# Performance work log

Hardware: AMD Instinct MI355X
Metric: run time of the kernel (lower is better)

The kernel has to match this reference:

```python
import jax, jax.numpy as jnp
import numpy as np

SR = 16000
FRAME_LENGTH = 2048
HOP = 512
WIN_LENGTH = 30
FREQ_LOW = 85
FREQ_HIGH = 3400
EPS = 1e-9


def setup_inputs() -> dict:
    key = jax.random.key(0)
    waveform = jax.random.normal(key, (8, 960000), dtype=jnp.float32)
    return {"waveform": waveform}


def _detect_pitch(w):
    # w: [B, T] padded waveform. Mirrors torchaudio.functional.detect_pitch_frequency.
    B, T = w.shape
    frame_size = int(np.ceil(SR * (HOP / SR)))          # = HOP = 512
    lags = int(np.ceil(SR / FREQ_LOW))                  # 189
    num_frames = int(np.ceil(T / frame_size))
    p = lags + num_frames * frame_size - T
    wp = jnp.pad(w, ((0, 0), (0, p)))                   # [B, lags + F*fs]
    frames = wp[:, : num_frames * frame_size].reshape(B, num_frames, frame_size)
    s1n = (EPS + jnp.linalg.norm(frames, axis=-1)) ** 2  # [B, F], lag-independent

    def body(carry, lag):
        seg = jax.lax.dynamic_slice_in_dim(wp, lag, num_frames * frame_size, axis=1)
        seg = seg.reshape(B, num_frames, frame_size)
        num = jnp.sum(frames * seg, axis=-1)
        s2n = (EPS + jnp.linalg.norm(seg, axis=-1)) ** 2
        return carry, num / s1n / s2n

    _, nccf = jax.lax.scan(body, None, jnp.arange(1, lags + 1))  # [lags, B, F]
    nccf = jnp.moveaxis(nccf, 0, -1)                             # [B, F, lags]

    # _find_max_per_frame
    lag_min = int(np.ceil(SR / FREQ_HIGH))  # 5
    half_size = lags // 2                   # 94
    best_v = jnp.max(nccf[..., lag_min:], axis=-1)
    best_i = jnp.argmax(nccf[..., lag_min:], axis=-1)
    half_v = jnp.max(nccf[..., lag_min:half_size], axis=-1)
    half_i = jnp.argmax(nccf[..., lag_min:half_size], axis=-1)
    mask = half_v > 0.99 * best_v           # prefer near-max with smallest lag
    idx = jnp.where(mask, half_i, best_i) + lag_min + 1  # +1 calibration offset

    # lower median (sorted index (n-1)//2). Output length = F - (WIN_LENGTH-1-pad_len).
    pad_len = (WIN_LENGTH - 1) // 2         # 14
    padded = jnp.concatenate([jnp.tile(idx[:, :1], (1, pad_len)), idx], axis=-1)
    out_len = padded.shape[-1] - WIN_LENGTH + 1
    win_idx = jnp.arange(out_len)[:, None] + jnp.arange(WIN_LENGTH)[None, :]
    wins = padded[:, win_idx]               # [B, out_len, WIN_LENGTH]
    med = jnp.sort(wins, axis=-1)[..., (WIN_LENGTH - 1) // 2]

    return SR / (EPS + med.astype(jnp.float32))


def reference(waveform):
    pad = FRAME_LENGTH // 2
    wpad = jnp.pad(waveform, ((0, 0), (pad, pad)), mode="reflect")
    pitch = _detect_pitch(wpad)
    desired = waveform.shape[-1] // HOP + 1
    if pitch.shape[-1] > desired:
        pitch = pitch[..., :desired]
    else:
        pitch = jnp.pad(pitch, ((0, 0), (0, desired - pitch.shape[-1])))
    return pitch
```

## Files before the change

kernel.cpp:

```cpp
#include <hip/hip_runtime.h>

#define T_WPAD  962048
#define T_RAW   960000
#define NFRM    1879
#define OUTW    1876
#define MEDLEN  1864
#define WINL    30
#define PADL    14
#define FPB     8
#define NBX     235
#define XLEN    4296

__global__ __launch_bounds__(256) void nccf_kernel(const float* __restrict__ wav,
                                                   int* __restrict__ idxArr) {
    const int bx   = blockIdx.x;
    const int b    = blockIdx.y;
    const int tid  = threadIdx.x;
    const int wave = tid >> 6;
    const int lane = tid & 63;
    const int h    = lane >> 5;
    const int s    = lane & 31;

    __shared__ __align__(16) float X[XLEN];
    __shared__ float Pw1[FPB][190];
    __shared__ float Pw2[FPB][190];

    const long a0 = (long)bx * (FPB * 512);
    const float* wrow = wav + (long)b * T_RAW;

    for (int i = tid; i < XLEN; i += 256) {
        float v = 0.0f;
        long t = a0 + i;
        if (t < T_WPAD) {
            long u = t - 1024;
            if (u < 0) u = -u;
            if (u >= T_RAW) u = 2L * (T_RAW - 1) - u;
            v = wrow[u];
        }
        X[i] = v;
    }
    __syncthreads();

    const int F = wave * 2 + h;
    const int g = bx * FPB + F;
    const bool valid = (g < NFRM);
    const float* Xf = X + F * 512;

    {
        const float* p = Xf + s * 22;
        double run = 0.0;
        #pragma unroll
        for (int m = 0; m < 22; ++m) { double x = (double)p[m]; run = fma(x, x, run); }
        double inc = run;
        #pragma unroll
        for (int off = 1; off < 32; off <<= 1) {
            double v = __shfl_up(inc, off, 32);
            if (s >= off) inc += v;
        }
        double run2 = inc - run;
        #pragma unroll
        for (int m = 0; m < 22; ++m) {
            double x = (double)p[m];
            run2 = fma(x, x, run2);
            int idx = s * 22 + m + 1;
            float val = (float)run2;
            if (idx <= 189)                     Pw1[F][idx - 1]   = val;
            else if (idx >= 512 && idx <= 701)  Pw2[F][idx - 512] = val;
        }
    }

    float acc[6] = {0.f, 0.f, 0.f, 0.f, 0.f, 0.f};
    {
        const float2* X2 = (const float2*)X;
        const int base2 = (F * 512 + 6 * s) >> 1;
        float w[12];
        #pragma unroll
        for (int d = 0; d < 6; ++d) {
            float2 t2 = X2[base2 + d];
            w[2 * d] = t2.x; w[2 * d + 1] = t2.y;
        }
        const float4* A4 = (const float4*)(X + F * 512);
        #pragma unroll 4
        for (int k = 0; k < 127; ++k) {
            float4 Av = A4[k];
            #pragma unroll
            for (int r = 0; r < 6; ++r) {
                acc[r] = fmaf(Av.x, w[1 + r], acc[r]);
                acc[r] = fmaf(Av.y, w[2 + r], acc[r]);
                acc[r] = fmaf(Av.z, w[3 + r], acc[r]);
                acc[r] = fmaf(Av.w, w[4 + r], acc[r]);
            }
            float2 n0 = X2[base2 + 2 * k + 6];
            float2 n1 = X2[base2 + 2 * k + 7];
            #pragma unroll
            for (int i = 0; i < 8; ++i) w[i] = w[i + 4];
            w[8] = n0.x; w[9] = n0.y; w[10] = n1.x; w[11] = n1.y;
        }
        {
            float4 Av = A4[127];
            #pragma unroll
            for (int r = 0; r < 6; ++r) {
                acc[r] = fmaf(Av.x, w[1 + r], acc[r]);
                acc[r] = fmaf(Av.y, w[2 + r], acc[r]);
                acc[r] = fmaf(Av.z, w[3 + r], acc[r]);
                acc[r] = fmaf(Av.w, w[4 + r], acc[r]);
            }
        }
    }

    float bestv = -1e30f, halfv = -1e30f;
    int bestk = 1 << 30, halfk = 1 << 30;
    {
        float s1 = 1e-9f + sqrtf(Pw2[F][0]);
        float s1n = s1 * s1;
        #pragma unroll
        for (int r = 0; r < 6; ++r) {
            int lag  = 6 * s + 1 + r;
            int kidx = lag - 1;
            if (kidx <= 188) {
                float q  = Pw2[F][lag] - Pw1[F][lag - 1];
                float s2 = 1e-9f + sqrtf(q);
                float v  = acc[r] / s1n / (s2 * s2);
                if (kidx >= 5) {
                    if (v > bestv) { bestv = v; bestk = kidx; }
                    if (kidx <= 93 && v > halfv) { halfv = v; halfk = kidx; }
                }
            }
        }
    }

    #pragma unroll
    for (int off = 16; off >= 1; off >>= 1) {
        float ov = __shfl_xor(bestv, off, 32); int ok = __shfl_xor(bestk, off, 32);
        if (ov > bestv || (ov == bestv && ok < bestk)) { bestv = ov; bestk = ok; }
        float hv = __shfl_xor(halfv, off, 32); int hk = __shfl_xor(halfk, off, 32);
        if (hv > halfv || (hv == halfv && hk < halfk)) { halfv = hv; halfk = hk; }
    }

    if (valid && s == 0) {
        bool m = (halfv > 0.99f * bestv);
        int sel = m ? halfk : bestk;
        idxArr[b * NFRM + g] = sel + 1;
    }
}

__global__ __launch_bounds__(256) void med_kernel(const int* __restrict__ idxArr,
                                                  float* __restrict__ out) {
    int gid = blockIdx.x * 256 + threadIdx.x;
    if (gid >= 8 * OUTW) return;
    int b = gid / OUTW;
    int i = gid - b * OUTW;
    float o = 0.0f;
    if (i < MEDLEN) {
        const int* row = idxArr + b * NFRM;
        int vals[WINL];
        #pragma unroll
        for (int m = 0; m < WINL; ++m) {
            int sIdx = i + m - PADL;
            vals[m] = row[sIdx < 0 ? 0 : sIdx];
        }
        int med = vals[0];
        #pragma unroll
        for (int c = 0; c < WINL; ++c) {
            int cl = 0, ce = 0;
            #pragma unroll
            for (int m = 0; m < WINL; ++m) {
                cl += (vals[m] <  vals[c]) ? 1 : 0;
                ce += (vals[m] == vals[c]) ? 1 : 0;
            }
            if (cl <= 14 && 14 < cl + ce) med = vals[c];
        }
        o = 16000.0f / (1e-9f + (float)med);
    }
    out[gid] = o;
}

extern "C" void kernel_launch(void* const* d_in, const int* in_sizes, int n_in,
                              void* d_out, int out_size, void* d_ws, size_t ws_size,
                              hipStream_t stream) {
    const float* wav = (const float*)d_in[0];
    float* out = (float*)d_out;
    int* idxArr = (int*)d_ws;

    dim3 gB(NBX, 8);
    hipLaunchKernelGGL(nccf_kernel, gB, dim3(256), 0, stream, wav, idxArr);

    int total = 8 * OUTW;
    hipLaunchKernelGGL(med_kernel, dim3((total + 255) / 256), dim3(256), 0, stream,
                       idxArr, out);
}
```

Baseline: 73.86 us.

## Use 16 frames per block, 12 lags per thread, vectorized interior loads

Each block now handles 16 frames, with 16 lanes per frame, so every thread computes 12 lags instead of 6. Each float4 of the frame loaded from shared memory is therefore reused across more accumulators, and the halo overhead per block shrinks. Interior blocks copy the waveform with float4 loads and no reflect-index arithmetic; edge blocks keep the scalar reflect path. The cost is more registers per thread, twice the LDS per block, fewer blocks in the grid, and a longer serial energy prefix scan per thread.

Result: faster. 72.00 us (-2.5%).

```diff
diff --git a/kernel.cpp b/kernel.cpp
--- a/kernel.cpp
+++ b/kernel.cpp
@@ -7,9 +7,10 @@
 #define MEDLEN  1864
 #define WINL    30
 #define PADL    14
-#define FPB     8
-#define NBX     235
-#define XLEN    4296
+#define FPB     16
+#define NBX     118
+#define XLEN    8392
+#define X4LEN   2098
 
 __global__ __launch_bounds__(256) void nccf_kernel(const float* __restrict__ wav,
                                                    int* __restrict__ idxArr) {
@@ -18,8 +19,8 @@
     const int tid  = threadIdx.x;
     const int wave = tid >> 6;
     const int lane = tid & 63;
-    const int h    = lane >> 5;
-    const int s    = lane & 31;
+    const int g    = lane >> 4;
+    const int s    = lane & 15;
 
     __shared__ __align__(16) float X[XLEN];
     __shared__ float Pw1[FPB][190];
@@ -28,83 +29,89 @@
     const long a0 = (long)bx * (FPB * 512);
     const float* wrow = wav + (long)b * T_RAW;
 
-    for (int i = tid; i < XLEN; i += 256) {
-        float v = 0.0f;
-        long t = a0 + i;
-        if (t < T_WPAD) {
-            long u = t - 1024;
-            if (u < 0) u = -u;
-            if (u >= T_RAW) u = 2L * (T_RAW - 1) - u;
-            v = wrow[u];
+    if (bx >= 1 && bx <= NBX - 2) {
+        const float4* src = (const float4*)(wrow + (a0 - 1024));
+        float4* dst = (float4*)X;
+        for (int i = tid; i < X4LEN; i += 256) dst[i] = src[i];
+    } else {
+        for (int i = tid; i < XLEN; i += 256) {
+            float v = 0.0f;
+            long t = a0 + i;
+            if (t < T_WPAD) {
+                long u = t - 1024;
+                if (u < 0) u = -u;
+                if (u >= T_RAW) u = 2L * (T_RAW - 1) - u;
+                v = wrow[u];
+            }
+            X[i] = v;
         }
-        X[i] = v;
     }
     __syncthreads();
 
-    const int F = wave * 2 + h;
-    const int g = bx * FPB + F;
-    const bool valid = (g < NFRM);
+    const int F  = wave * 4 + g;
+    const int gf = bx * FPB + F;
+    const bool valid = (gf < NFRM);
     const float* Xf = X + F * 512;
 
     {
-        const float* p = Xf + s * 22;
+        const float* p = Xf + s * 44;
         double run = 0.0;
         #pragma unroll
-        for (int m = 0; m < 22; ++m) { double x = (double)p[m]; run = fma(x, x, run); }
+        for (int m = 0; m < 44; ++m) { double x = (double)p[m]; run = fma(x, x, run); }
         double inc = run;
         #pragma unroll
-        for (int off = 1; off < 32; off <<= 1) {
-            double v = __shfl_up(inc, off, 32);
+        for (int off = 1; off < 16; off <<= 1) {
+            double v = __shfl_up(inc, off, 16);
             if (s >= off) inc += v;
         }
         double run2 = inc - run;
         #pragma unroll
-        for (int m = 0; m < 22; ++m) {
+        for (int m = 0; m < 44; ++m) {
             double x = (double)p[m];
             run2 = fma(x, x, run2);
-            int idx = s * 22 + m + 1;
+            int idx = s * 44 + m + 1;
             float val = (float)run2;
             if (idx <= 189)                     Pw1[F][idx - 1]   = val;
             else if (idx >= 512 && idx <= 701)  Pw2[F][idx - 512] = val;
         }
     }
 
-    float acc[6] = {0.f, 0.f, 0.f, 0.f, 0.f, 0.f};
+    float acc[12];
+    #pragma unroll
+    for (int r = 0; r < 12; ++r) acc[r] = 0.0f;
     {
-        const float2* X2 = (const float2*)X;
-        const int base2 = (F * 512 + 6 * s) >> 1;
-        float w[12];
+        const float4* X4 = (const float4*)X;
+        const int aBase = F * 128;
+        const int wBase = aBase + 3 * s;
+        float w[16];
         #pragma unroll
-        for (int d = 0; d < 6; ++d) {
-            float2 t2 = X2[base2 + d];
-            w[2 * d] = t2.x; w[2 * d + 1] = t2.y;
+        for (int d = 0; d < 4; ++d) {
+            float4 t4 = X4[wBase + d];
+            w[4 * d] = t4.x; w[4 * d + 1] = t4.y; w[4 * d + 2] = t4.z; w[4 * d + 3] = t4.w;
         }
-        const float4* A4 = (const float4*)(X + F * 512);
+        float4 A = X4[aBase];
         #pragma unroll 4
         for (int k = 0; k < 127; ++k) {
-            float4 Av = A4[k];
+            float4 An = X4[aBase + k + 1];
+            float4 nx = X4[wBase + k + 4];
             #pragma unroll
-            for (int r = 0; r < 6; ++r) {
-                acc[r] = fmaf(Av.x, w[1 + r], acc[r]);
-                acc[r] = fmaf(Av.y, w[2 + r], acc[r]);
-                acc[r] = fmaf(Av.z, w[3 + r], acc[r]);
-                acc[r] = fmaf(Av.w, w[4 + r], acc[r]);
+            for (int r = 0; r < 12; ++r) {
+                acc[r] = fmaf(A.x, w[r + 1], acc[r]);
+                acc[r] = fmaf(A.y, w[r + 2], acc[r]);
+                acc[r] = fmaf(A.z, w[r + 3], acc[r]);
+                acc[r] = fmaf(A.w, w[r + 4], acc[r]);
             }
-            float2 n0 = X2[base2 + 2 * k + 6];
-            float2 n1 = X2[base2 + 2 * k + 7];
             #pragma unroll
-            for (int i = 0; i < 8; ++i) w[i] = w[i + 4];
-            w[8] = n0.x; w[9] = n0.y; w[10] = n1.x; w[11] = n1.y;
+            for (int i = 0; i < 12; ++i) w[i] = w[i + 4];
+            w[12] = nx.x; w[13] = nx.y; w[14] = nx.z; w[15] = nx.w;
+            A = An;
         }
-        {
-            float4 Av = A4[127];
-            #pragma unroll
-            for (int r = 0; r < 6; ++r) {
-                acc[r] = fmaf(Av.x, w[1 + r], acc[r]);
-                acc[r] = fmaf(Av.y, w[2 + r], acc[r]);
-                acc[r] = fmaf(Av.z, w[3 + r], acc[r]);
-                acc[r] = fmaf(Av.w, w[4 + r], acc[r]);
-            }
+        #pragma unroll
+        for (int r = 0; r < 12; ++r) {
+            acc[r] = fmaf(A.x, w[r + 1], acc[r]);
+            acc[r] = fmaf(A.y, w[r + 2], acc[r]);
+            acc[r] = fmaf(A.z, w[r + 3], acc[r]);
+            acc[r] = fmaf(A.w, w[r + 4], acc[r]);
         }
     }
 
@@ -114,13 +121,13 @@
         float s1 = 1e-9f + sqrtf(Pw2[F][0]);
         float s1n = s1 * s1;
         #pragma unroll
-        for (int r = 0; r < 6; ++r) {
-            int lag  = 6 * s + 1 + r;
+        for (int r = 1; r <= 12; ++r) {
+            int lag  = 12 * s + r;
             int kidx = lag - 1;
             if (kidx <= 188) {
                 float q  = Pw2[F][lag] - Pw1[F][lag - 1];
                 float s2 = 1e-9f + sqrtf(q);
-                float v  = acc[r] / s1n / (s2 * s2);
+                float v  = acc[r - 1] / s1n / (s2 * s2);
                 if (kidx >= 5) {
                     if (v > bestv) { bestv = v; bestk = kidx; }
                     if (kidx <= 93 && v > halfv) { halfv = v; halfk = kidx; }
@@ -130,17 +137,17 @@
     }
 
     #pragma unroll
-    for (int off = 16; off >= 1; off >>= 1) {
-        float ov = __shfl_xor(bestv, off, 32); int ok = __shfl_xor(bestk, off, 32);
+    for (int off = 8; off >= 1; off >>= 1) {
+        float ov = __shfl_xor(bestv, off, 16); int ok = __shfl_xor(bestk, off, 16);
         if (ov > bestv || (ov == bestv && ok < bestk)) { bestv = ov; bestk = ok; }
-        float hv = __shfl_xor(halfv, off, 32); int hk = __shfl_xor(halfk, off, 32);
+        float hv = __shfl_xor(halfv, off, 16); int hk = __shfl_xor(halfk, off, 16);
         if (hv > halfv || (hv == halfv && hk < halfk)) { halfv = hv; halfk = hk; }
     }
 
     if (valid && s == 0) {
         bool m = (halfv > 0.99f * bestv);
         int sel = m ? halfk : bestk;
-        idxArr[b * NFRM + g] = sel + 1;
+        idxArr[b * NFRM + gf] = sel + 1;
     }
 }
 
```
